# Kernel optimization log

Hardware: AMD Instinct MI355X
Metric: run time of the kernel (lower is better)

The kernel has to match this reference:

```python
import jax, jax.numpy as jnp
import numpy as np

REL_DIM = 64
HIDDEN = 128
IN_DIM = 7  # dist, dx, dy, color_diff(3), size_diff(1)


def setup_inputs() -> dict:
    key = jax.random.key(0)
    ks = jax.random.split(key, 8)
    B, N = 4, 512
    pos = jax.random.normal(ks[0], (B, N, 2), dtype=jnp.float32)
    color = jax.random.uniform(ks[1], (B, N, 3), dtype=jnp.float32)
    size = jax.random.uniform(ks[2], (B, N, 1), dtype=jnp.float32)
    # MLP params: Linear(7,128) -> GELU -> Linear(128,64), torch default init scale
    W1 = jax.random.normal(ks[3], (IN_DIM, HIDDEN), dtype=jnp.float32) / np.sqrt(IN_DIM)
    b1 = jax.random.normal(ks[4], (HIDDEN,), dtype=jnp.float32) * 0.01
    W2 = jax.random.normal(ks[5], (HIDDEN, REL_DIM), dtype=jnp.float32) / np.sqrt(HIDDEN)
    b2 = jax.random.normal(ks[6], (REL_DIM,), dtype=jnp.float32) * 0.01
    return {"pos": pos, "color": color, "size": size,
            "W1": W1, "b1": b1, "W2": W2, "b2": b2}


def reference(pos, color, size, W1, b1, W2, b2):
    # pos: (B,N,2), color: (B,N,3), size: (B,N,1)
    dx = pos[:, :, None, 0] - pos[:, None, :, 0]          # (B,N,N)
    dy = pos[:, :, None, 1] - pos[:, None, :, 1]          # (B,N,N)
    dist = jnp.sqrt(dx * dx + dy * dy + 1e-6)             # (B,N,N)
    color_diff = color[:, :, None, :] - color[:, None, :, :]  # (B,N,N,3)
    size_diff = size[:, :, None, :] - size[:, None, :, :]     # (B,N,N,1)
    geom = jnp.concatenate(
        [dist[..., None], dx[..., None], dy[..., None], color_diff, size_diff],
        axis=-1)                                          # (B,N,N,7)
    h = jax.nn.gelu(jnp.einsum('bijc,ch->bijh', geom, W1) + b1, approximate=False)
    rel = jnp.einsum('bijh,hr->bijr', h, W2) + b2          # (B,N,N,rel_dim)
    return rel
```

## Files before the change

kernel.cpp:

```cpp
#include <hip/hip_runtime.h>
#include <math.h>

#define NPTS 512
#define HID 128
#define RELD 64

typedef __attribute__((ext_vector_type(8))) short short8;
typedef __attribute__((ext_vector_type(4))) float f32x4;
typedef __attribute__((ext_vector_type(4))) int i32x4;

__global__ __launch_bounds__(256) void prep_tables(
    const float* __restrict__ pos, const float* __restrict__ color,
    const float* __restrict__ size, const float* __restrict__ W1,
    const float* __restrict__ b1, float* __restrict__ ui,
    unsigned short* __restrict__ uj, int npts)
{
  const int g = blockIdx.x * blockDim.x + threadIdx.x;
  const int k = g & (HID - 1), p = g >> 7;
  float v = pos[p * 2 + 0] * W1[1 * HID + k];
  v = fmaf(pos[p * 2 + 1], W1[2 * HID + k], v);
  v = fmaf(color[p * 3 + 0], W1[3 * HID + k], v);
  v = fmaf(color[p * 3 + 1], W1[4 * HID + k], v);
  v = fmaf(color[p * 3 + 2], W1[5 * HID + k], v);
  v = fmaf(size[p], W1[6 * HID + k], v);
  ui[g] = v + b1[k];
  const __bf16 vb = (__bf16)v;
  uj[((size_t)(k >> 3) * npts + p) * 8 + (k & 7)] = __builtin_bit_cast(unsigned short, vb);
}

__global__ __launch_bounds__(256) void relgeom_mfma3(
    const float* __restrict__ pos, const float* __restrict__ W1,
    const float* __restrict__ ui, const unsigned short* __restrict__ uj,
    const float* __restrict__ W2, const float* __restrict__ b2,
    float* __restrict__ out, int npts)
{
  __shared__ __align__(16) char lds[16384 + 4 * 4096];
  const int tid = threadIdx.x;
  const int lane = tid & 63, wid = tid >> 6;
  const int l15 = lane & 15, lq = lane >> 4, l3 = lane & 3;

#pragma unroll
  for (int n = 0; n < 32; ++n) {
    const int m = tid + 256 * n;
    const int k = m >> 6, r = m & 63;
    const __bf16 wb = (__bf16)W2[m];
    *(__bf16*)(lds + r * 256 + (((k >> 3) ^ (r & 7)) << 4) + (k & 7) * 2) = wb;
  }
  __syncthreads();

  const int bx = blockIdx.x;
  const int i  = (bx >> 1) & (NPTS - 1);
  const int b  = bx >> 10;
  const int pi = b * NPTS + i;
  const int j  = ((bx & 1) << 8) + tid;
  const int pj = b * NPTS + j;

  const float dx = pos[pi * 2 + 0] - pos[pj * 2 + 0];
  const float dy = pos[pi * 2 + 1] - pos[pj * 2 + 1];
  const float dist = sqrtf(fmaf(dx, dx, fmaf(dy, dy, 1e-6f)));

  const float* __restrict__ uirow = ui + (size_t)pi * HID;
  const float* __restrict__ w1d = W1;

  f32x4 acc[4][4];
#pragma unroll
  for (int rt = 0; rt < 4; ++rt) {
    const f32x4 bb = *(const f32x4*)(b2 + rt * 16 + lq * 4);
#pragma unroll
    for (int pt = 0; pt < 4; ++pt) acc[rt][pt] = bb;
  }

  char* const hbase = lds + 16384 + wid * 4096;

  for (int ks = 0; ks < 4; ++ks) {
    union { i32x4 v[4]; unsigned u[16]; } U;
#pragma unroll
    for (int d = 0; d < 4; ++d)
      U.v[d] = *(const i32x4*)(uj + ((size_t)(ks * 4 + d) * npts + pj) * 8);

    union { short s[32]; i32x4 v[4]; } hb;
#pragma unroll
    for (int kk = 0; kk < 32; ++kk) {
      const int k = ks * 32 + kk;
      const unsigned w = U.u[kk >> 1];
      const float ujf = __builtin_bit_cast(float, (kk & 1) ? (w & 0xffff0000u) : (w << 16));
      float h = fmaf(dist, w1d[k], uirow[k] - ujf);
      const float h2 = h * h;
      const float wq = fmaf(h2, -0.1029534f, -2.3022077f);
      const float ex = __builtin_amdgcn_exp2f(h * wq);
      const float gel = h * __builtin_amdgcn_rcpf(1.0f + ex);
      const __bf16 hbf = (__bf16)gel;
      hb.s[kk] = __builtin_bit_cast(short, hbf);
    }
#pragma unroll
    for (int d = 0; d < 4; ++d)
      *(i32x4*)(hbase + lane * 64 + ((d ^ l3) << 4)) = hb.v[d];

    short8 afr[4];
#pragma unroll
    for (int rt = 0; rt < 4; ++rt) {
      const int r = rt * 16 + l15;
      afr[rt] = *(const short8*)(lds + r * 256 + (((ks * 4 + lq) ^ (r & 7)) << 4));
    }
#pragma unroll
    for (int pt = 0; pt < 4; ++pt) {
      const int p = pt * 16 + l15;
      const short8 bfr = *(const short8*)(hbase + p * 64 + ((lq ^ (p & 3)) << 4));
#pragma unroll
      for (int rt = 0; rt < 4; ++rt)
        acc[rt][pt] = __builtin_amdgcn_mfma_f32_16x16x32_bf16(afr[rt], bfr, acc[rt][pt], 0, 0, 0);
    }
  }

  const int pbase = bx * 256 + wid * 64;
#pragma unroll
  for (int pt = 0; pt < 4; ++pt)
#pragma unroll
    for (int rt = 0; rt < 4; ++rt)
      *(f32x4*)(out + (size_t)(pbase + pt * 16 + l15) * RELD + rt * 16 + lq * 4) = acc[rt][pt];
}

__global__ __launch_bounds__(256) void relgeom_mfma_fb(
    const float* __restrict__ pos, const float* __restrict__ color,
    const float* __restrict__ size, const float* __restrict__ W1,
    const float* __restrict__ b1, const float* __restrict__ W2,
    const float* __restrict__ b2, float* __restrict__ out)
{
  __shared__ __align__(16) char lds[16384 + 4 * 4096];
  const int tid = threadIdx.x;
  const int lane = tid & 63;
  const int wid = tid >> 6;
  const int l15 = lane & 15, lq = lane >> 4, l3 = lane & 3;
#pragma unroll
  for (int n = 0; n < 32; ++n) {
    const int m = tid + 256 * n;
    const int k = m >> 6, r = m & 63;
    const __bf16 wb = (__bf16)W2[m];
    *(__bf16*)(lds + r * 256 + (((k >> 3) ^ (r & 7)) << 4) + (k & 7) * 2) = wb;
  }
  __syncthreads();
  const int pbase = (blockIdx.x * 4 + wid) * 64;
  const int t = pbase + lane;
  const int j = t & (NPTS - 1);
  const int bi = t >> 9;
  const int i = bi & (NPTS - 1);
  const int b = bi >> 9;
  const int pi = b * NPTS + i, pj = b * NPTS + j;
  const float dx = pos[pi * 2 + 0] - pos[pj * 2 + 0];
  const float dy = pos[pi * 2 + 1] - pos[pj * 2 + 1];
  const float g0 = sqrtf(fmaf(dx, dx, fmaf(dy, dy, 1e-6f)));
  const float g3 = color[pi * 3 + 0] - color[pj * 3 + 0];
  const float g4 = color[pi * 3 + 1] - color[pj * 3 + 1];
  const float g5 = color[pi * 3 + 2] - color[pj * 3 + 2];
  const float g6 = size[pi] - size[pj];
  f32x4 acc[4][4];
#pragma unroll
  for (int nt = 0; nt < 4; ++nt) {
    const float bb = b2[nt * 16 + l15];
#pragma unroll
    for (int s = 0; s < 4; ++s) acc[s][nt] = (f32x4){bb, bb, bb, bb};
  }
  char* const hbase = lds + 16384 + wid * 4096;
  for (int ks = 0; ks < 4; ++ks) {
    union { short s[32]; i32x4 v[4]; } hb;
#pragma unroll
    for (int kk = 0; kk < 32; ++kk) {
      const int k = ks * 32 + kk;
      float h = b1[k];
      h = fmaf(g0, W1[0 * HID + k], h);
      h = fmaf(dx, W1[1 * HID + k], h);
      h = fmaf(dy, W1[2 * HID + k], h);
      h = fmaf(g3, W1[3 * HID + k], h);
      h = fmaf(g4, W1[4 * HID + k], h);
      h = fmaf(g5, W1[5 * HID + k], h);
      h = fmaf(g6, W1[6 * HID + k], h);
      const float h2 = h * h;
      const float wq = fmaf(h2, -0.1029534f, -2.3022077f);
      const float ex = __builtin_amdgcn_exp2f(h * wq);
      const float gel = h * __builtin_amdgcn_rcpf(1.0f + ex);
      const __bf16 hbf = (__bf16)gel;
      hb.s[kk] = __builtin_bit_cast(short, hbf);
    }
#pragma unroll
    for (int d = 0; d < 4; ++d)
      *(i32x4*)(hbase + lane * 64 + ((d ^ l3) << 4)) = hb.v[d];
    short8 bfr[4];
#pragma unroll
    for (int nt = 0; nt < 4; ++nt) {
      const int r = nt * 16 + l15;
      bfr[nt] = *(const short8*)(lds + r * 256 + (((ks * 4 + lq) ^ (r & 7)) << 4));
    }
#pragma unroll
    for (int s = 0; s < 4; ++s) {
      const short8 af = *(const short8*)(hbase + (s * 16 + l15) * 64 + ((lq ^ l3) << 4));
#pragma unroll
      for (int nt = 0; nt < 4; ++nt)
        acc[s][nt] = __builtin_amdgcn_mfma_f32_16x16x32_bf16(af, bfr[nt], acc[s][nt], 0, 0, 0);
    }
  }
  float* const op = out + (size_t)pbase * RELD;
#pragma unroll
  for (int s = 0; s < 4; ++s)
#pragma unroll
    for (int nt = 0; nt < 4; ++nt)
#pragma unroll
      for (int ri = 0; ri < 4; ++ri)
        op[(s * 16 + lq * 4 + ri) * RELD + nt * 16 + l15] = acc[s][nt][ri];
}

extern "C" void kernel_launch(void* const* d_in, const int* in_sizes, int n_in,
                              void* d_out, int out_size, void* d_ws, size_t ws_size,
                              hipStream_t stream) {
  const float* pos   = (const float*)d_in[0];
  const float* color = (const float*)d_in[1];
  const float* size  = (const float*)d_in[2];
  const float* W1    = (const float*)d_in[3];
  const float* b1    = (const float*)d_in[4];
  const float* W2    = (const float*)d_in[5];
  const float* b2    = (const float*)d_in[6];
  float* out = (float*)d_out;

  const int B = in_sizes[0] / (NPTS * 2);
  const int npts = B * NPTS;
  const long long pairs = (long long)B * NPTS * NPTS;
  const int grid = (int)(pairs / 256);

  const size_t ui_bytes = (size_t)npts * HID * sizeof(float);
  const size_t uj_bytes = (size_t)npts * HID * sizeof(unsigned short);

  if (ws_size >= ui_bytes + uj_bytes) {
    float* ui = (float*)d_ws;
    unsigned short* uj = (unsigned short*)((char*)d_ws + ui_bytes);
    prep_tables<<<npts * HID / 256, 256, 0, stream>>>(pos, color, size, W1, b1, ui, uj, npts);
    relgeom_mfma3<<<grid, 256, 0, stream>>>(pos, W1, ui, uj, W2, b2, out, npts);
  } else {
    relgeom_mfma_fb<<<grid, 256, 0, stream>>>(pos, color, size, W1, b1, W2, b2, out);
  }
}
```

Measured before the change: 86.40 us.

## Compute GELU activations directly in MFMA fragment layout, skip LDS staging

Each lane now computes the hidden activations for exactly the elements it feeds into the MFMA B operand (8 k-values for two pair columns), eliminating the per-wave LDS write/read of the activation tile. Blocks now cover 128 pairs with 32 per wave, halving LDS usage and accumulator registers to raise occupancy. In exchange the grid doubles, so the W2-to-LDS preload is repeated twice as often and weight fragments are reused across fewer pair tiles.

```diff
diff --git a/kernel.cpp b/kernel.cpp
--- a/kernel.cpp
+++ b/kernel.cpp
@@ -28,16 +28,16 @@
   uj[((size_t)(k >> 3) * npts + p) * 8 + (k & 7)] = __builtin_bit_cast(unsigned short, vb);
 }
 
-__global__ __launch_bounds__(256) void relgeom_mfma3(
+__global__ __launch_bounds__(256) void relgeom_mfma4(
     const float* __restrict__ pos, const float* __restrict__ W1,
     const float* __restrict__ ui, const unsigned short* __restrict__ uj,
     const float* __restrict__ W2, const float* __restrict__ b2,
     float* __restrict__ out, int npts)
 {
-  __shared__ __align__(16) char lds[16384 + 4 * 4096];
+  __shared__ __align__(16) char lds[16384];
   const int tid = threadIdx.x;
   const int lane = tid & 63, wid = tid >> 6;
-  const int l15 = lane & 15, lq = lane >> 4, l3 = lane & 3;
+  const int l15 = lane & 15, lq = lane >> 4;
 
 #pragma unroll
   for (int n = 0; n < 32; ++n) {
@@ -49,75 +49,77 @@
   __syncthreads();
 
   const int bx = blockIdx.x;
-  const int i  = (bx >> 1) & (NPTS - 1);
-  const int b  = bx >> 10;
+  const int i  = (bx >> 2) & (NPTS - 1);
+  const int b  = bx >> 11;
   const int pi = b * NPTS + i;
-  const int j  = ((bx & 1) << 8) + tid;
-  const int pj = b * NPTS + j;
-
-  const float dx = pos[pi * 2 + 0] - pos[pj * 2 + 0];
-  const float dy = pos[pi * 2 + 1] - pos[pj * 2 + 1];
-  const float dist = sqrtf(fmaf(dx, dx, fmaf(dy, dy, 1e-6f)));
+  const int jbase = ((bx & 3) << 7) + (wid << 5);
+  const int pj0 = b * NPTS + jbase + l15;
+  const int pj1 = pj0 + 16;
+
+  const float pix = pos[pi * 2 + 0], piy = pos[pi * 2 + 1];
+  const float dx0 = pix - pos[pj0 * 2 + 0], dy0 = piy - pos[pj0 * 2 + 1];
+  const float dx1 = pix - pos[pj1 * 2 + 0], dy1 = piy - pos[pj1 * 2 + 1];
+  const float dist0 = sqrtf(fmaf(dx0, dx0, fmaf(dy0, dy0, 1e-6f)));
+  const float dist1 = sqrtf(fmaf(dx1, dx1, fmaf(dy1, dy1, 1e-6f)));
 
   const float* __restrict__ uirow = ui + (size_t)pi * HID;
-  const float* __restrict__ w1d = W1;
-
-  f32x4 acc[4][4];
+
+  f32x4 acc[4][2];
 #pragma unroll
   for (int rt = 0; rt < 4; ++rt) {
     const f32x4 bb = *(const f32x4*)(b2 + rt * 16 + lq * 4);
-#pragma unroll
-    for (int pt = 0; pt < 4; ++pt) acc[rt][pt] = bb;
-  }
-
-  char* const hbase = lds + 16384 + wid * 4096;
-
+    acc[rt][0] = bb;
+    acc[rt][1] = bb;
+  }
+
+#pragma unroll
   for (int ks = 0; ks < 4; ++ks) {
-    union { i32x4 v[4]; unsigned u[16]; } U;
-#pragma unroll
-    for (int d = 0; d < 4; ++d)
-      U.v[d] = *(const i32x4*)(uj + ((size_t)(ks * 4 + d) * npts + pj) * 8);
-
-    union { short s[32]; i32x4 v[4]; } hb;
-#pragma unroll
-    for (int kk = 0; kk < 32; ++kk) {
-      const int k = ks * 32 + kk;
-      const unsigned w = U.u[kk >> 1];
-      const float ujf = __builtin_bit_cast(float, (kk & 1) ? (w & 0xffff0000u) : (w << 16));
-      float h = fmaf(dist, w1d[k], uirow[k] - ujf);
-      const float h2 = h * h;
-      const float wq = fmaf(h2, -0.1029534f, -2.3022077f);
-      const float ex = __builtin_amdgcn_exp2f(h * wq);
-      const float gel = h * __builtin_amdgcn_rcpf(1.0f + ex);
-      const __bf16 hbf = (__bf16)gel;
-      hb.s[kk] = __builtin_bit_cast(short, hbf);
-    }
-#pragma unroll
-    for (int d = 0; d < 4; ++d)
-      *(i32x4*)(hbase + lane * 64 + ((d ^ l3) << 4)) = hb.v[d];
-
-    short8 afr[4];
+    const int kofs = ks * 32 + lq * 8;
+    const f32x4 uiA = *(const f32x4*)(uirow + kofs);
+    const f32x4 uiB = *(const f32x4*)(uirow + kofs + 4);
+    const f32x4 w1A = *(const f32x4*)(W1 + kofs);
+    const f32x4 w1B = *(const f32x4*)(W1 + kofs + 4);
+    const int o = ks * 4 + lq;
+    union { i32x4 v; unsigned u[4]; } uj0, uj1;
+    uj0.v = *(const i32x4*)(uj + ((size_t)o * npts + pj0) * 8);
+    uj1.v = *(const i32x4*)(uj + ((size_t)o * npts + pj1) * 8);
+
+    short8 bfr0, bfr1;
+#pragma unroll
+    for (int e = 0; e < 8; ++e) {
+      const float uiv = (e < 4) ? uiA[e] : uiB[e - 4];
+      const float w1v = (e < 4) ? w1A[e] : w1B[e - 4];
+#pragma unroll
+      for (int pt = 0; pt < 2; ++pt) {
+        const unsigned w = pt ? uj1.u[e >> 1] : uj0.u[e >> 1];
+        const float ujf = __builtin_bit_cast(float, (e & 1) ? (w & 0xffff0000u) : (w << 16));
+        const float dist = pt ? dist1 : dist0;
+        const float h = fmaf(dist, w1v, uiv - ujf);
+        const float h2 = h * h;
+        const float wq = fmaf(h2, -0.1029534f, -2.3022077f);
+        const float ex = __builtin_amdgcn_exp2f(h * wq);
+        const float gel = h * __builtin_amdgcn_rcpf(1.0f + ex);
+        const __bf16 hbf = (__bf16)gel;
+        if (pt) bfr1[e] = __builtin_bit_cast(short, hbf);
+        else    bfr0[e] = __builtin_bit_cast(short, hbf);
+      }
+    }
+
 #pragma unroll
     for (int rt = 0; rt < 4; ++rt) {
       const int r = rt * 16 + l15;
-      afr[rt] = *(const short8*)(lds + r * 256 + (((ks * 4 + lq) ^ (r & 7)) << 4));
-    }
-#pragma unroll
-    for (int pt = 0; pt < 4; ++pt) {
-      const int p = pt * 16 + l15;
-      const short8 bfr = *(const short8*)(hbase + p * 64 + ((lq ^ (p & 3)) << 4));
-#pragma unroll
-      for (int rt = 0; rt < 4; ++rt)
-        acc[rt][pt] = __builtin_amdgcn_mfma_f32_16x16x32_bf16(afr[rt], bfr, acc[rt][pt], 0, 0, 0);
-    }
-  }
-
-  const int pbase = bx * 256 + wid * 64;
-#pragma unroll
-  for (int pt = 0; pt < 4; ++pt)
+      const short8 af = *(const short8*)(lds + r * 256 + ((o ^ (r & 7)) << 4));
+      acc[rt][0] = __builtin_amdgcn_mfma_f32_16x16x32_bf16(af, bfr0, acc[rt][0], 0, 0, 0);
+      acc[rt][1] = __builtin_amdgcn_mfma_f32_16x16x32_bf16(af, bfr1, acc[rt][1], 0, 0, 0);
+    }
+  }
+
+  const size_t orow = ((size_t)pi * NPTS + jbase);
+#pragma unroll
+  for (int pt = 0; pt < 2; ++pt)
 #pragma unroll
     for (int rt = 0; rt < 4; ++rt)
-      *(f32x4*)(out + (size_t)(pbase + pt * 16 + l15) * RELD + rt * 16 + lq * 4) = acc[rt][pt];
+      *(f32x4*)(out + (orow + pt * 16 + l15) * RELD + rt * 16 + lq * 4) = acc[rt][pt];
 }
 
 __global__ __launch_bounds__(256) void relgeom_mfma_fb(
@@ -223,7 +225,6 @@
   const int B = in_sizes[0] / (NPTS * 2);
   const int npts = B * NPTS;
   const long long pairs = (long long)B * NPTS * NPTS;
-  const int grid = (int)(pairs / 256);
 
   const size_t ui_bytes = (size_t)npts * HID * sizeof(float);
   const size_t uj_bytes = (size_t)npts * HID * sizeof(unsigned short);
@@ -232,8 +233,9 @@
     float* ui = (float*)d_ws;
     unsigned short* uj = (unsigned short*)((char*)d_ws + ui_bytes);
     prep_tables<<<npts * HID / 256, 256, 0, stream>>>(pos, color, size, W1, b1, ui, uj, npts);
-    relgeom_mfma3<<<grid, 256, 0, stream>>>(pos, W1, ui, uj, W2, b2, out, npts);
+    const int grid = (int)(pairs / 128);
+    relgeom_mfma4<<<grid, 256, 0, stream>>>(pos, W1, ui, uj, W2, b2, out, npts);
   } else {
-    relgeom_mfma_fb<<<grid, 256, 0, stream>>>(pos, color, size, W1, b1, W2, b2, out);
-  }
-}
+    relgeom_mfma_fb<<<(int)(pairs / 256), 256, 0, stream>>>(pos, color, size, W1, b1, W2, b2, out);
+  }
+}
```

After: 91.23 us. 1.06x slower.
